# Kernel optimization log

Hardware: AMD Instinct MI355X
Metric: run time of the kernel (lower is better)

The kernel has to match this reference:

```python
import jax, jax.numpy as jnp
import numpy as np
from jax import lax

N, C, H, W = 16, 1, 512, 512
MAX_ITERS = H + W  # upper bound on flood-fill propagation distance


def _dilate4(r):
    # 3x3 cross (4-connectivity) grayscale dilation, r: (N,H,W)
    rp = jnp.pad(r, ((0, 0), (1, 1), (1, 1)))
    up = rp[:, :-2, 1:-1]
    dn = rp[:, 2:, 1:-1]
    lf = rp[:, 1:-1, :-2]
    rt = rp[:, 1:-1, 2:]
    return jnp.maximum(jnp.maximum(jnp.maximum(up, dn), jnp.maximum(lf, rt)), r)


def _reconstruct_dilation(marker, mask):
    # skimage.morphology.reconstruction(seed, mask, method='dilation'):
    # iterate rec = min(dilate(rec), mask) until convergence.
    def cond(state):
        _, changed, i = state
        return jnp.logical_and(changed, i < MAX_ITERS)

    def body(state):
        r, _, i = state
        nr = jnp.minimum(_dilate4(r), mask)
        return nr, jnp.any(nr != r), i + 1

    rec, _, _ = lax.while_loop(cond, body, (marker, jnp.array(True), jnp.array(0)))
    return rec


def _adaptive_binarize(prob, marker_factor, mask_factor):
    # prob: (N,1,H,W); mirrors torch .detach() -> threshold -> reconstruction
    img = lax.stop_gradient(prob[:, 0])  # (N,H,W)
    nzm = img > 0
    cnt = jnp.sum(nzm, axis=(1, 2))                      # (N,)
    safe = jnp.maximum(cnt, 1).astype(img.dtype)
    mean = jnp.sum(jnp.where(nzm, img, 0.0), axis=(1, 2)) / safe
    var = jnp.sum(jnp.where(nzm, (img - mean[:, None, None]) ** 2, 0.0), axis=(1, 2)) / safe
    std = jnp.sqrt(var)

    def threshold(factor):
        T = (mean + factor * std)[:, None, None]
        b = img > T
        empty = jnp.sum(b, axis=(1, 2)) == 0
        T2 = (mean + (factor / 2.0) * std)[:, None, None]
        b2 = img > T2
        return jnp.where(empty[:, None, None], b2, b)

    marker = threshold(marker_factor).astype(jnp.float32)
    maskb = threshold(mask_factor).astype(jnp.float32)
    rec = _reconstruct_dilation(marker, maskb)
    out = (rec > 0.5).astype(jnp.float32)
    out = jnp.where((cnt == 0)[:, None, None], 0.0, out)  # no nonzero pixels -> zeros
    return out[:, None]  # (N,1,H,W)


def setup_inputs() -> dict:
    key = jax.random.key(0)
    k1, k2 = jax.random.split(key)
    thick_logit = jax.random.normal(k1, (N, C, H, W), dtype=jnp.float32)
    thin_logit = jax.random.normal(k2, (N, C, H, W), dtype=jnp.float32)
    return {"thick_logit": thick_logit, "thin_logit": thin_logit}


def reference(thick_logit, thin_logit):
    thick_prob = jax.nn.sigmoid(thick_logit)
    thin_prob = jax.nn.sigmoid(thin_logit)
    thick_bin = _adaptive_binarize(thick_prob, 2.0, 0.5)
    thin_bin = _adaptive_binarize(thin_prob, 4.0, 0.5)
    fused_bin = jnp.clip(thick_bin + thin_bin, 0.0, 1.0)
    return thick_logit, thin_logit, fused_bin
```

## Files before the change

kernel.cpp:

```cpp
#include <hip/hip_runtime.h>
#include <cstdint>
#include <cstddef>

#define HW 512
#define NPIX (HW * HW)
#define NIMG 16
#define NII 32
#define CHUNKS 64
#define CHUNK_PIX 4096
#define IN_ELEMS (NIMG * NPIX)
#define WPI 4096

typedef unsigned long long u64;

#define WS_PARTA 0u
#define WS_ZM    65536u
#define WS_MSEL  98304u
#define WS_KSEL  (WS_MSEL + 1048576u)
#define WS_ROUT  (WS_KSEL + 1048576u)

__device__ __forceinline__ float sigmoid_f32(float x) {
    return (float)(1.0 / (1.0 + exp(-(double)x)));
}

__device__ __forceinline__ float sigmoid_fast(float xf) {
    double x = (double)xf;
    double y = x * -1.4426950408889634074;
    if (y > 1000.0)  return 0.0f;
    if (y < -1000.0) return 1.0f;
    double n = __builtin_rint(y);
    double t = (y - n) * 0.69314718055994530942;
    double p = 2.5052108385441718775e-8;
    p = __builtin_fma(p, t, 2.7557319223985890653e-7);
    p = __builtin_fma(p, t, 2.7557319223985892511e-6);
    p = __builtin_fma(p, t, 2.4801587301587301566e-5);
    p = __builtin_fma(p, t, 1.9841269841269841253e-4);
    p = __builtin_fma(p, t, 1.3888888888888889419e-3);
    p = __builtin_fma(p, t, 8.3333333333333332177e-3);
    p = __builtin_fma(p, t, 4.1666666666666664354e-2);
    p = __builtin_fma(p, t, 1.6666666666666665741e-1);
    p = __builtin_fma(p, t, 5.0e-1);
    p = __builtin_fma(p, t, 1.0);
    p = __builtin_fma(p, t, 1.0);
    long long bits = ((long long)n + 1023ll) << 52;
    double e = p * __longlong_as_double(bits);
    double d = 1.0 + e;
    if (y > 100.0 || y < -100.0)
        return (float)(1.0 / d);
    double r = (double)__builtin_amdgcn_rcpf((float)d);
    r = r * (2.0 - d * r);
    r = r * (2.0 - d * r);
    return (float)r;
}

__global__ void k1_copy_stats(const float* __restrict__ A, const float* __restrict__ B,
                              float* __restrict__ out, double* __restrict__ partA) {
    int b = blockIdx.x;
    int ii = b >> 6, chunk = b & 63;
    int j = ii >> 4, n = ii & 15;
    const float* src = (j == 0 ? A : B) + (size_t)n * NPIX + (size_t)chunk * CHUNK_PIX;
    float* dst = out + (size_t)j * IN_ELEMS + (size_t)n * NPIX + (size_t)chunk * CHUNK_PIX;

    double s = 0.0, sq = 0.0, cc = 0.0;
    float mx = -__builtin_inff();
#pragma unroll
    for (int p = 0; p < 4; ++p) {
        float4 v = *(const float4*)(src + p * 1024 + threadIdx.x * 4);
        *(float4*)(dst + p * 1024 + threadIdx.x * 4) = v;
        float xs[4] = {v.x, v.y, v.z, v.w};
#pragma unroll
        for (int q = 0; q < 4; ++q) {
            float img = sigmoid_fast(xs[q]);
            mx = fmaxf(mx, xs[q]);
            if (img > 0.0f) { double d = (double)img; s += d; sq += d * d; cc += 1.0; }
        }
    }
    __shared__ double sm[256], sv[256], sc[256];
    __shared__ float smx[256];
    sm[threadIdx.x] = s; sv[threadIdx.x] = sq; sc[threadIdx.x] = cc; smx[threadIdx.x] = mx;
    __syncthreads();
    for (int off = 128; off > 0; off >>= 1) {
        if (threadIdx.x < off) {
            sm[threadIdx.x] += sm[threadIdx.x + off];
            sv[threadIdx.x] += sv[threadIdx.x + off];
            sc[threadIdx.x] += sc[threadIdx.x + off];
            smx[threadIdx.x] = fmaxf(smx[threadIdx.x], smx[threadIdx.x + off]);
        }
        __syncthreads();
    }
    if (threadIdx.x == 0) {
        double* p = partA + (size_t)(ii * 64 + chunk) * 4;
        p[0] = sm[0]; p[1] = sv[0]; p[2] = sc[0]; p[3] = (double)smx[0];
    }
}

__device__ __forceinline__ float key_to_f32(unsigned k) {
    unsigned b = (k & 0x80000000u) ? (k ^ 0x80000000u) : ~k;
    return __uint_as_float(b);
}
__device__ float find_cut(double T) {
    if (!(1.0 > T)) return __uint_as_float(0x7F800000u);
    unsigned lo = 0x007FFFFFu;
    unsigned hi = 0xFF800000u;
    while (lo < hi) {
        unsigned mid = lo + ((hi - lo) >> 1);
        float x = key_to_f32(mid);
        float s32 = sigmoid_f32(x);
        if ((double)s32 > T) hi = mid; else lo = mid + 1;
    }
    return key_to_f32(lo);
}

__global__ void k2_bits(const float* __restrict__ A, const float* __restrict__ B,
                        const double* __restrict__ partA,
                        u64* __restrict__ msel, u64* __restrict__ ksel,
                        u64* __restrict__ zm) {
    int b = blockIdx.x, ii = b >> 6, chunk = b & 63;
    int j = ii >> 4, n = ii & 15;
    const float* src = (j == 0 ? A : B) + (size_t)n * NPIX;
    int t = threadIdx.x, lane = t & 63, w = t >> 6;

    __shared__ double shst[4];
    __shared__ float cs[4];
    __shared__ float cut2[2];

    if (t < 64) {
        const double* p = partA + (size_t)(ii * 64 + t) * 4;
        double s = p[0], sq = p[1], c = p[2], mx = p[3];
#pragma unroll
        for (int off = 32; off > 0; off >>= 1) {
            s  += __shfl_down(s,  (unsigned)off, 64);
            sq += __shfl_down(sq, (unsigned)off, 64);
            c  += __shfl_down(c,  (unsigned)off, 64);
            mx  = fmax(mx, __shfl_down(mx, (unsigned)off, 64));
        }
        if (t == 0) {
            double mean = 0.0, sd = 0.0;
            if (c > 0.0) {
                mean = s / c;
                double var = sq / c - mean * mean;
                if (var < 0.0) var = 0.0;
                sd = sqrt(var);
            }
            shst[0] = mean; shst[1] = sd; shst[2] = c; shst[3] = mx;
        }
    }
    __syncthreads();
    if (t < 4) {
        double mean = shst[0], sd = shst[1];
        double fac = (ii < 16) ? 2.0 : 4.0;
        double T = (t == 0) ? mean + fac * sd
                 : (t == 1) ? mean + 0.5 * fac * sd
                 : (t == 2) ? mean + 0.5 * sd
                 :            mean + 0.25 * sd;
        cs[t] = find_cut(T);
    }
    __syncthreads();
    if (t == 0) {
        float mxf = (float)shst[3];
        cut2[0] = (mxf >= cs[0]) ? cs[0] : cs[1];
        cut2[1] = (mxf >= cs[2]) ? cs[2] : cs[3];
        if (chunk == 0) zm[ii] = (shst[2] > 0.0) ? ~0ull : 0ull;
    }
    __syncthreads();
    float cM = cut2[0], cK = cut2[1];

#pragma unroll 4
    for (int i = 0; i < 16; ++i) {
        float x = src[chunk * CHUNK_PIX + i * 256 + t];
        u64 bM = __ballot(x >= cM);
        u64 bK = __ballot(x >= cK);
        if (lane == 0) {
            size_t g = (size_t)ii * WPI + (size_t)chunk * 64 + i * 4 + w;
            msel[g] = bM; ksel[g] = bK;
        }
    }
}

__device__ __forceinline__ void hfill8(u64* x, const u64* k) {
    u64 c = 0;
#pragma unroll
    for (int w = 0; w < 8; ++w) {
        u64 a = k[w], g = x[w];
        u64 t1 = a + g;  u64 c1 = (u64)(t1 < a);
        u64 t2 = t1 + c; u64 c2 = (u64)(t2 < t1);
        c = c1 | c2;
        x[w] = (~t2 | g) & a;
    }
    c = 0;
#pragma unroll
    for (int w = 7; w >= 0; --w) {
        u64 a = __brevll(k[w]), g = __brevll(x[w]);
        u64 t1 = a + g;  u64 c1 = (u64)(t1 < a);
        u64 t2 = t1 + c; u64 c2 = (u64)(t2 < t1);
        c = c1 | c2;
        x[w] = __brevll((~t2 | g) & a);
    }
}

__global__ __launch_bounds__(512) void k3_flood(const u64* __restrict__ msel,
                                                const u64* __restrict__ ksel,
                                                u64* __restrict__ rout) {
    int ii = blockIdx.x, t = threadIdx.x;
    __shared__ u64 R[8 * HW];
    const u64* M = msel + (size_t)ii * WPI;
    const u64* K = ksel + (size_t)ii * WPI;

    u64 r[8], k[8];
#pragma unroll
    for (int w = 0; w < 8; ++w) {
        k[w] = K[(size_t)t * 8 + w];
        r[w] = M[(size_t)t * 8 + w] & k[w];
    }
    hfill8(r, k);
#pragma unroll
    for (int w = 0; w < 8; ++w) R[w * HW + t] = r[w];
    __syncthreads();

    for (int round = 0; round < 256; ++round) {
        u64 gained = 0;
#pragma unroll 1
        for (int sweep = 0; sweep < 4; ++sweep) {
            u64 diff = 0;
#pragma unroll
            for (int w = 0; w < 8; ++w) {
                u64 nb = (t > 0      ? R[w * HW + (t - 1)] : 0ull)
                       | (t < HW - 1 ? R[w * HW + (t + 1)] : 0ull);
                u64 g = nb & k[w] & ~r[w];
                r[w] |= g; diff |= g;
            }
            if (diff) {
                hfill8(r, k);
#pragma unroll
                for (int w = 0; w < 8; ++w) R[w * HW + t] = r[w];
                gained |= diff;
            }
            asm volatile("" ::: "memory");
        }
        if (!__syncthreads_or(gained != 0ull ? 1 : 0)) break;
    }

#pragma unroll
    for (int w = 0; w < 8; ++w)
        rout[(size_t)ii * WPI + (size_t)w * HW + t] = r[w];
}

__global__ void k4_fuse(const u64* __restrict__ rout,
                        const u64* __restrict__ zm,
                        float* __restrict__ out) {
    size_t gid = (size_t)blockIdx.x * blockDim.x + threadIdx.x;
    size_t p = gid * 4;
    int n = (int)(p >> 18);
    int e = (int)(p & (NPIX - 1));
    size_t gw = (size_t)(((e >> 6) & 7) * HW + (e >> 9));
    u64 w = (rout[(size_t)n * WPI + gw] & zm[n])
          | (rout[(size_t)(16 + n) * WPI + gw] & zm[16 + n]);
    int sh = e & 63;
    float4 v;
    v.x = ((w >> sh) & 1ull)       ? 1.0f : 0.0f;
    v.y = ((w >> (sh + 1)) & 1ull) ? 1.0f : 0.0f;
    v.z = ((w >> (sh + 2)) & 1ull) ? 1.0f : 0.0f;
    v.w = ((w >> (sh + 3)) & 1ull) ? 1.0f : 0.0f;
    *(float4*)(out + 2 * (size_t)IN_ELEMS + p) = v;
}

extern "C" void kernel_launch(void* const* d_in, const int* in_sizes, int n_in,
                              void* d_out, int out_size, void* d_ws, size_t ws_size,
                              hipStream_t stream) {
    const float* A = (const float*)d_in[0];
    const float* B = (const float*)d_in[1];
    float* out = (float*)d_out;
    char* ws = (char*)d_ws;

    double* partA = (double*)(ws + WS_PARTA);
    u64*    zm    = (u64*)(ws + WS_ZM);
    u64*    msel  = (u64*)(ws + WS_MSEL);
    u64*    ksel  = (u64*)(ws + WS_KSEL);
    u64*    rout  = (u64*)(ws + WS_ROUT);

    k1_copy_stats<<<NII * CHUNKS, 256, 0, stream>>>(A, B, out, partA);
    k2_bits<<<NII * CHUNKS, 256, 0, stream>>>(A, B, partA, msel, ksel, zm);
    k3_flood<<<NII, 512, 0, stream>>>(msel, ksel, rout);
    k4_fuse<<<4096, 256, 0, stream>>>(rout, zm, out);
}
```

Measured before the change: 142.7 us.

## Add banded pre-flood kernel to propagate within 64-row bands before full flood

Adds a new kernel that splits each image into 8 bands of 64 rows, one 64-thread block per band, and runs the flood fill inside each band until it converges or hits a round cap. The result is written back into the marker buffer, so the existing whole-image flood kernel starts from a marker that is already mostly filled and should need fewer serial iterations. This spreads work across 256 blocks instead of 32 and so uses more of the GPU, at the cost of an extra launch and an extra read and write of the bitmaps. Results stay correct because the band fill is a monotone subset of the full reconstruction. The in-band sweeps rely on wavefront-synchronous shared-memory reads without a barrier, which is safe here because each 64-thread block is a single wavefront on this hardware.

```diff
diff --git a/kernel.cpp b/kernel.cpp
--- a/kernel.cpp
+++ b/kernel.cpp
@@ -198,6 +198,55 @@
     }
 }
 
+__global__ __launch_bounds__(64) void k3a_band(u64* __restrict__ msel,
+                                               const u64* __restrict__ ksel) {
+    int b = blockIdx.x;
+    int ii = b >> 3, band = b & 7;
+    int t = threadIdx.x;
+    int row = band * 64 + t;
+    __shared__ u64 R[8 * 64];
+    const u64* M = msel + (size_t)ii * WPI;
+    const u64* K = ksel + (size_t)ii * WPI;
+
+    u64 r[8], k[8];
+#pragma unroll
+    for (int w = 0; w < 8; ++w) {
+        k[w] = K[(size_t)row * 8 + w];
+        r[w] = M[(size_t)row * 8 + w] & k[w];
+    }
+    hfill8(r, k);
+#pragma unroll
+    for (int w = 0; w < 8; ++w) R[w * 64 + t] = r[w];
+    __syncthreads();
+
+    for (int round = 0; round < 24; ++round) {
+        u64 gained = 0;
+#pragma unroll 1
+        for (int sweep = 0; sweep < 4; ++sweep) {
+            u64 diff = 0;
+#pragma unroll
+            for (int w = 0; w < 8; ++w) {
+                u64 nb = (t > 0  ? R[w * 64 + (t - 1)] : 0ull)
+                       | (t < 63 ? R[w * 64 + (t + 1)] : 0ull);
+                u64 g = nb & k[w] & ~r[w];
+                r[w] |= g; diff |= g;
+            }
+            if (diff) {
+                hfill8(r, k);
+#pragma unroll
+                for (int w = 0; w < 8; ++w) R[w * 64 + t] = r[w];
+                gained |= diff;
+            }
+            asm volatile("" ::: "memory");
+        }
+        if (!__syncthreads_or(gained != 0ull ? 1 : 0)) break;
+    }
+
+#pragma unroll
+    for (int w = 0; w < 8; ++w)
+        msel[(size_t)ii * WPI + (size_t)row * 8 + w] = r[w];
+}
+
 __global__ __launch_bounds__(512) void k3_flood(const u64* __restrict__ msel,
                                                 const u64* __restrict__ ksel,
                                                 u64* __restrict__ rout) {
@@ -280,6 +329,7 @@
 
     k1_copy_stats<<<NII * CHUNKS, 256, 0, stream>>>(A, B, out, partA);
     k2_bits<<<NII * CHUNKS, 256, 0, stream>>>(A, B, partA, msel, ksel, zm);
+    k3a_band<<<NII * 8, 64, 0, stream>>>(msel, ksel);
     k3_flood<<<NII, 512, 0, stream>>>(msel, ksel, rout);
     k4_fuse<<<4096, 256, 0, stream>>>(rout, zm, out);
 }
```

Result: slower. 152.2 us (+6.7%).

## Fuse flood-fill and output expansion into one kernel per image pair

Applied to the files above, without the earlier changes.

Merges the flood kernel and the fuse kernel into one launch. Each 1024-thread block floods both the thick and thin images for one batch index in shared memory, then writes the float output directly from shared memory. This removes the rout global round trip and one launch. In exchange it halves the number of flood blocks, couples the convergence of the two images through one sync, and does the large output write from only 16 blocks.

```diff
diff --git a/kernel.cpp b/kernel.cpp
--- a/kernel.cpp
+++ b/kernel.cpp
@@ -17,7 +17,6 @@
 #define WS_ZM    65536u
 #define WS_MSEL  98304u
 #define WS_KSEL  (WS_MSEL + 1048576u)
-#define WS_ROUT  (WS_KSEL + 1048576u)
 
 __device__ __forceinline__ float sigmoid_f32(float x) {
     return (float)(1.0 / (1.0 + exp(-(double)x)));
@@ -198,23 +197,29 @@
     }
 }
 
-__global__ __launch_bounds__(512) void k3_flood(const u64* __restrict__ msel,
-                                                const u64* __restrict__ ksel,
-                                                u64* __restrict__ rout) {
-    int ii = blockIdx.x, t = threadIdx.x;
-    __shared__ u64 R[8 * HW];
+__global__ __launch_bounds__(1024) void k3k4_flood_fuse(const u64* __restrict__ msel,
+                                                        const u64* __restrict__ ksel,
+                                                        const u64* __restrict__ zm,
+                                                        float* __restrict__ out) {
+    int n = blockIdx.x;
+    int t = threadIdx.x;
+    int img = t >> 9;
+    int row = t & 511;
+    int ii = img * 16 + n;
+    __shared__ u64 R[2][8 * HW];
+    u64* Ri = R[img];
     const u64* M = msel + (size_t)ii * WPI;
     const u64* K = ksel + (size_t)ii * WPI;
 
     u64 r[8], k[8];
 #pragma unroll
     for (int w = 0; w < 8; ++w) {
-        k[w] = K[(size_t)t * 8 + w];
-        r[w] = M[(size_t)t * 8 + w] & k[w];
+        k[w] = K[(size_t)row * 8 + w];
+        r[w] = M[(size_t)row * 8 + w] & k[w];
     }
     hfill8(r, k);
 #pragma unroll
-    for (int w = 0; w < 8; ++w) R[w * HW + t] = r[w];
+    for (int w = 0; w < 8; ++w) Ri[w * HW + row] = r[w];
     __syncthreads();
 
     for (int round = 0; round < 256; ++round) {
@@ -224,44 +229,39 @@
             u64 diff = 0;
 #pragma unroll
             for (int w = 0; w < 8; ++w) {
-                u64 nb = (t > 0      ? R[w * HW + (t - 1)] : 0ull)
-                       | (t < HW - 1 ? R[w * HW + (t + 1)] : 0ull);
+                u64 nb = (row > 0      ? Ri[w * HW + (row - 1)] : 0ull)
+                       | (row < HW - 1 ? Ri[w * HW + (row + 1)] : 0ull);
                 u64 g = nb & k[w] & ~r[w];
                 r[w] |= g; diff |= g;
             }
             if (diff) {
                 hfill8(r, k);
 #pragma unroll
-                for (int w = 0; w < 8; ++w) R[w * HW + t] = r[w];
+                for (int w = 0; w < 8; ++w) Ri[w * HW + row] = r[w];
                 gained |= diff;
             }
             asm volatile("" ::: "memory");
         }
         if (!__syncthreads_or(gained != 0ull ? 1 : 0)) break;
     }
-
-#pragma unroll
-    for (int w = 0; w < 8; ++w)
-        rout[(size_t)ii * WPI + (size_t)w * HW + t] = r[w];
-}
-
-__global__ void k4_fuse(const u64* __restrict__ rout,
-                        const u64* __restrict__ zm,
-                        float* __restrict__ out) {
-    size_t gid = (size_t)blockIdx.x * blockDim.x + threadIdx.x;
-    size_t p = gid * 4;
-    int n = (int)(p >> 18);
-    int e = (int)(p & (NPIX - 1));
-    size_t gw = (size_t)(((e >> 6) & 7) * HW + (e >> 9));
-    u64 w = (rout[(size_t)n * WPI + gw] & zm[n])
-          | (rout[(size_t)(16 + n) * WPI + gw] & zm[16 + n]);
-    int sh = e & 63;
-    float4 v;
-    v.x = ((w >> sh) & 1ull)       ? 1.0f : 0.0f;
-    v.y = ((w >> (sh + 1)) & 1ull) ? 1.0f : 0.0f;
-    v.z = ((w >> (sh + 2)) & 1ull) ? 1.0f : 0.0f;
-    v.w = ((w >> (sh + 3)) & 1ull) ? 1.0f : 0.0f;
-    *(float4*)(out + 2 * (size_t)IN_ELEMS + p) = v;
+    __syncthreads();
+
+    u64 zm0 = zm[n], zm1 = zm[16 + n];
+    float* dst = out + 2 * (size_t)IN_ELEMS + (size_t)n * NPIX;
+#pragma unroll 4
+    for (int i = 0; i < 64; ++i) {
+        int p4 = i * 1024 + t;
+        int e = p4 * 4;
+        int gw = ((e >> 6) & 7) * HW + (e >> 9);
+        u64 w = (R[0][gw] & zm0) | (R[1][gw] & zm1);
+        int sh = e & 63;
+        float4 v;
+        v.x = ((w >> sh) & 1ull)       ? 1.0f : 0.0f;
+        v.y = ((w >> (sh + 1)) & 1ull) ? 1.0f : 0.0f;
+        v.z = ((w >> (sh + 2)) & 1ull) ? 1.0f : 0.0f;
+        v.w = ((w >> (sh + 3)) & 1ull) ? 1.0f : 0.0f;
+        *(float4*)(dst + e) = v;
+    }
 }
 
 extern "C" void kernel_launch(void* const* d_in, const int* in_sizes, int n_in,
@@ -276,10 +276,8 @@
     u64*    zm    = (u64*)(ws + WS_ZM);
     u64*    msel  = (u64*)(ws + WS_MSEL);
     u64*    ksel  = (u64*)(ws + WS_KSEL);
-    u64*    rout  = (u64*)(ws + WS_ROUT);
 
     k1_copy_stats<<<NII * CHUNKS, 256, 0, stream>>>(A, B, out, partA);
     k2_bits<<<NII * CHUNKS, 256, 0, stream>>>(A, B, partA, msel, ksel, zm);
-    k3_flood<<<NII, 512, 0, stream>>>(msel, ksel, rout);
-    k4_fuse<<<4096, 256, 0, stream>>>(rout, zm, out);
-}
+    k3k4_flood_fuse<<<NIMG, 1024, 0, stream>>>(msel, ksel, zm, out);
+}
```

Measured after the change: 159.3 us. 1.12x slower.

## Give each flood-fill thread four rows and propagate between them in registers

Applied to the files above, without the earlier changes.

The flood kernel now uses 128 threads per image instead of 512, and each thread holds four consecutive rows in registers. Vertical propagation between a thread's own rows runs in registers through a down-then-up pass. Only the top and bottom rows are exchanged through shared memory, which cuts shared-memory traffic and speeds intra-thread propagation per sweep. In exchange, register pressure and serial work per thread rise, and fewer waves are available to hide latency.

```diff
diff --git a/kernel.cpp b/kernel.cpp
--- a/kernel.cpp
+++ b/kernel.cpp
@@ -198,51 +198,88 @@
     }
 }
 
-__global__ __launch_bounds__(512) void k3_flood(const u64* __restrict__ msel,
+__global__ __launch_bounds__(128) void k3_flood(const u64* __restrict__ msel,
                                                 const u64* __restrict__ ksel,
                                                 u64* __restrict__ rout) {
     int ii = blockIdx.x, t = threadIdx.x;
-    __shared__ u64 R[8 * HW];
+    __shared__ u64 Rt[8 * 128];
+    __shared__ u64 Rb[8 * 128];
     const u64* M = msel + (size_t)ii * WPI;
     const u64* K = ksel + (size_t)ii * WPI;
 
-    u64 r[8], k[8];
+    u64 r0[8], r1[8], r2[8], r3[8], k0[8], k1[8], k2[8], k3[8];
 #pragma unroll
     for (int w = 0; w < 8; ++w) {
-        k[w] = K[(size_t)t * 8 + w];
-        r[w] = M[(size_t)t * 8 + w] & k[w];
-    }
-    hfill8(r, k);
-#pragma unroll
-    for (int w = 0; w < 8; ++w) R[w * HW + t] = r[w];
+        k0[w] = K[(size_t)(4 * t + 0) * 8 + w];
+        k1[w] = K[(size_t)(4 * t + 1) * 8 + w];
+        k2[w] = K[(size_t)(4 * t + 2) * 8 + w];
+        k3[w] = K[(size_t)(4 * t + 3) * 8 + w];
+        r0[w] = M[(size_t)(4 * t + 0) * 8 + w] & k0[w];
+        r1[w] = M[(size_t)(4 * t + 1) * 8 + w] & k1[w];
+        r2[w] = M[(size_t)(4 * t + 2) * 8 + w] & k2[w];
+        r3[w] = M[(size_t)(4 * t + 3) * 8 + w] & k3[w];
+    }
+    hfill8(r0, k0); hfill8(r1, k1); hfill8(r2, k2); hfill8(r3, k3);
+#pragma unroll
+    for (int w = 0; w < 8; ++w) { Rt[w * 128 + t] = r0[w]; Rb[w * 128 + t] = r3[w]; }
     __syncthreads();
 
     for (int round = 0; round < 256; ++round) {
         u64 gained = 0;
 #pragma unroll 1
         for (int sweep = 0; sweep < 4; ++sweep) {
-            u64 diff = 0;
+            u64 dT = 0, dB = 0, d1 = 0, d2 = 0, dBc = 0, d2u = 0, d1u = 0, dTu = 0;
 #pragma unroll
             for (int w = 0; w < 8; ++w) {
-                u64 nb = (t > 0      ? R[w * HW + (t - 1)] : 0ull)
-                       | (t < HW - 1 ? R[w * HW + (t + 1)] : 0ull);
-                u64 g = nb & k[w] & ~r[w];
-                r[w] |= g; diff |= g;
-            }
-            if (diff) {
-                hfill8(r, k);
-#pragma unroll
-                for (int w = 0; w < 8; ++w) R[w * HW + t] = r[w];
-                gained |= diff;
-            }
+                u64 nb = (t > 0) ? Rb[w * 128 + (t - 1)] : 0ull;
+                u64 g = nb & k0[w] & ~r0[w]; r0[w] |= g; dT |= g;
+            }
+#pragma unroll
+            for (int w = 0; w < 8; ++w) {
+                u64 nb = (t < 127) ? Rt[w * 128 + (t + 1)] : 0ull;
+                u64 g = nb & k3[w] & ~r3[w]; r3[w] |= g; dB |= g;
+            }
+            if (dT) hfill8(r0, k0);
+#pragma unroll
+            for (int w = 0; w < 8; ++w) { u64 g = r0[w] & k1[w] & ~r1[w]; r1[w] |= g; d1 |= g; }
+            if (d1) hfill8(r1, k1);
+#pragma unroll
+            for (int w = 0; w < 8; ++w) { u64 g = r1[w] & k2[w] & ~r2[w]; r2[w] |= g; d2 |= g; }
+            if (d2) hfill8(r2, k2);
+#pragma unroll
+            for (int w = 0; w < 8; ++w) { u64 g = r2[w] & k3[w] & ~r3[w]; r3[w] |= g; dBc |= g; }
+            if (dB | dBc) hfill8(r3, k3);
+#pragma unroll
+            for (int w = 0; w < 8; ++w) { u64 g = r3[w] & k2[w] & ~r2[w]; r2[w] |= g; d2u |= g; }
+            if (d2u) hfill8(r2, k2);
+#pragma unroll
+            for (int w = 0; w < 8; ++w) { u64 g = r2[w] & k1[w] & ~r1[w]; r1[w] |= g; d1u |= g; }
+            if (d1u) hfill8(r1, k1);
+#pragma unroll
+            for (int w = 0; w < 8; ++w) { u64 g = r1[w] & k0[w] & ~r0[w]; r0[w] |= g; dTu |= g; }
+            if (dTu) hfill8(r0, k0);
+            if (dT | dTu) {
+#pragma unroll
+                for (int w = 0; w < 8; ++w) Rt[w * 128 + t] = r0[w];
+            }
+            if (dB | dBc) {
+#pragma unroll
+                for (int w = 0; w < 8; ++w) Rb[w * 128 + t] = r3[w];
+            }
+            gained |= dT | dB | d1 | d2 | dBc | d2u | d1u | dTu;
             asm volatile("" ::: "memory");
         }
         if (!__syncthreads_or(gained != 0ull ? 1 : 0)) break;
     }
 
 #pragma unroll
-    for (int w = 0; w < 8; ++w)
-        rout[(size_t)ii * WPI + (size_t)w * HW + t] = r[w];
+    for (int w = 0; w < 8; ++w) {
+        u64* dst = rout + (size_t)ii * WPI + (size_t)w * HW + (size_t)(4 * t);
+        ulonglong2 lo, hi;
+        lo.x = r0[w]; lo.y = r1[w]; hi.x = r2[w]; hi.y = r3[w];
+        *(ulonglong2*)(dst)     = lo;
+        *(ulonglong2*)(dst + 2) = hi;
+    }
 }
 
 __global__ void k4_fuse(const u64* __restrict__ rout,
@@ -280,6 +317,6 @@
 
     k1_copy_stats<<<NII * CHUNKS, 256, 0, stream>>>(A, B, out, partA);
     k2_bits<<<NII * CHUNKS, 256, 0, stream>>>(A, B, partA, msel, ksel, zm);
-    k3_flood<<<NII, 512, 0, stream>>>(msel, ksel, rout);
+    k3_flood<<<NII, 128, 0, stream>>>(msel, ksel, rout);
     k4_fuse<<<4096, 256, 0, stream>>>(rout, zm, out);
 }
```

After: 153.0 us. 7.2% more time.
